# Kernel optimization log

Measured on AMD Instinct MI355X. Metric: run time of the kernel, lower is better.

Reference implementation:

```python
import jax, jax.numpy as jnp
import numpy as np

B = 2048; N_UP = 8; N_DN = 8; N_EL = 16; N_ION = 4
DF_EE = 4; DF_EI = 4; DF_II = 4; D_EL = 32; D_ION = 32
W_EDGE = 64; D_NODE = 128; CUTOFF = 5.0  # cutoff_distance, cutoff_type='exponential'


def setup_inputs() -> dict:
    key = jax.random.key(0)
    keys = iter(jax.random.split(key, 64))
    nk = lambda: next(keys)
    W = lambda fi, fo: jax.random.normal(nk(), (fi, fo), jnp.float32) / np.float32(np.sqrt(fi))
    b = lambda fo: jnp.zeros((fo,), jnp.float32)
    inp = {}
    inp["feat_el"] = jax.random.normal(nk(), (B, N_EL, D_EL), jnp.float32)
    inp["feat_el_el"] = jax.random.normal(nk(), (B, N_EL, N_EL, DF_EE), jnp.float32)
    inp["feat_el_ion"] = jax.random.normal(nk(), (B, N_EL, N_ION, DF_EI), jnp.float32)
    inp["feat_ion"] = jax.random.normal(nk(), (N_ION, D_ION), jnp.float32)
    inp["feat_ion_ion"] = jax.random.normal(nk(), (N_ION, N_ION, DF_II), jnp.float32)
    inp["dist_el_el"] = jax.random.uniform(nk(), (B, N_EL, N_EL), jnp.float32) * 6.0 + 0.1
    inp["dist_el_ion"] = jax.random.uniform(nk(), (B, N_EL, N_ION), jnp.float32) * 6.0 + 0.1
    # 2-layer edge MLPs: el_ion, same-spin, diff-spin, ion_ion
    for p, fi in (("ei", DF_EI), ("sa", DF_EE), ("di", DF_EE), ("io", DF_II)):
        inp["W" + p + "0"] = W(fi, W_EDGE); inp["b" + p + "0"] = b(W_EDGE)
        inp["W" + p + "1"] = W(W_EDGE, W_EDGE); inp["b" + p + "1"] = b(W_EDGE)
    # el_ion message-passing layer
    inp["Ws_ei"] = W(D_ION, W_EDGE); inp["bs_ei"] = b(W_EDGE)
    inp["Wu_ei"] = W(D_EL + W_EDGE, D_NODE); inp["bu_ei"] = b(D_NODE)
    inp["We_ei"] = W(W_EDGE, W_EDGE); inp["be_ei"] = b(W_EDGE)
    # el_el dense GNN, 2 iterations
    for i in ("0", "1"):
        inp["Ws" + i] = W(D_NODE, W_EDGE); inp["bs" + i] = b(W_EDGE)
        inp["Wu" + i] = W(D_NODE + W_EDGE, D_NODE); inp["bu" + i] = b(D_NODE)
        inp["We" + i] = W(W_EDGE, W_EDGE); inp["be" + i] = b(W_EDGE)
    inp["n_up"] = N_UP
    return inp


def _mlp2(x, W0, b0, W1, b1):
    # MLP with linear_out=False -> activation on every layer
    return jnp.tanh(jnp.tanh(x @ W0 + b0) @ W1 + b1)


def _mp(x_r, x_s, e, mask, Ws, bs, Wu, bu, We, be):
    # Message passing: edge * projected-sender messages, masked sum over senders,
    # node update from [receiver, aggregated msg]; edge update by linear+tanh.
    s = jnp.tanh(x_s @ Ws + bs)                      # [..., n_s, De]
    msg = e * s[..., None, :, :] * mask[..., None]   # [..., n_r, n_s, De]
    agg = msg.sum(axis=-2)                           # [..., n_r, De]
    x_new = jnp.tanh(jnp.concatenate([x_r, agg], axis=-1) @ Wu + bu)
    e_new = jnp.tanh(e @ We + be)
    return x_new, e_new


def reference(feat_el, feat_el_el, feat_el_ion, feat_ion, feat_ion_ion, dist_el_el, dist_el_ion,
              Wei0, bei0, Wei1, bei1, Wsa0, bsa0, Wsa1, bsa1, Wdi0, bdi0, Wdi1, bdi1,
              Wio0, bio0, Wio1, bio1, Ws_ei, bs_ei, Wu_ei, bu_ei, We_ei, be_ei,
              Ws0, bs0, Wu0, bu0, We0, be0, Ws1, bs1, Wu1, bu1, We1, be1, n_up):
    n_el = feat_el.shape[-2]; n_dn = n_el - n_up
    bd = feat_el_el.shape[:-3]
    ee = feat_el_el
    # --- _embed_edges: slice el-el pairs into same/diff spin blocks ---
    up_up = ee[..., :n_up, :n_up, :].reshape(bd + (n_up * n_up, -1))
    up_dn = ee[..., :n_up, n_up:, :].reshape(bd + (n_up * n_dn, -1))
    dn_up = ee[..., n_up:, :n_up, :].reshape(bd + (n_dn * n_up, -1))
    dn_dn = ee[..., n_up:, n_up:, :].reshape(bd + (n_dn * n_dn, -1))
    same = _mlp2(jnp.concatenate([up_up, dn_dn], axis=-2), Wsa0, bsa0, Wsa1, bsa1)
    diff = _mlp2(jnp.concatenate([up_dn, dn_up], axis=-2), Wdi0, bdi0, Wdi1, bdi1)
    edge_el_ion = _mlp2(feat_el_ion, Wei0, bei0, Wei1, bei1)
    _edge_ion_ion = _mlp2(feat_ion_ion, Wio0, bio0, Wio1, bio1)  # unused when ion_gnn='none' (as in original)
    # --- reassemble el-el edges ---
    up_up = same[..., : n_up * n_up, :].reshape(bd + (n_up, n_up, -1))
    dn_dn = same[..., n_up * n_up :, :].reshape(bd + (n_dn, n_dn, -1))
    up_dn = diff[..., : n_up * n_dn, :].reshape(bd + (n_up, n_dn, -1))
    dn_up = diff[..., n_up * n_dn :, :].reshape(bd + (n_dn, n_up, -1))
    edge_el_el = jnp.concatenate([
        jnp.concatenate([up_up, up_dn], axis=-2),
        jnp.concatenate([dn_up, dn_dn], axis=-2)], axis=-3)
    # --- distance masks (cutoff_type='exponential') ---
    mask_ei = jnp.exp(-dist_el_ion / CUTOFF)
    mask_ee = jnp.exp(-dist_el_el / CUTOFF)
    # --- ion_gnn='none': emb_ion = raw ion features ---
    emb_ion = feat_ion
    # --- el-ion message passing, then 2-iteration dense el-el GNN ---
    emb_el, edge_el_ion = _mp(feat_el, emb_ion, edge_el_ion, mask_ei, Ws_ei, bs_ei, Wu_ei, bu_ei, We_ei, be_ei)
    emb_el, edge_el_el = _mp(emb_el, emb_el, edge_el_el, mask_ee, Ws0, bs0, Wu0, bu0, We0, be0)
    emb_el, edge_el_el = _mp(emb_el, emb_el, edge_el_el, mask_ee, Ws1, bs1, Wu1, bu1, We1, be1)
    return emb_el, feat_ion, edge_el_el, edge_el_ion
```

## Files before the change

### kernel.cpp

```cpp
#include <hip/hip_runtime.h>

typedef unsigned short u16;
typedef unsigned int u32;
typedef __attribute__((ext_vector_type(4))) unsigned int u32x4;
typedef __attribute__((ext_vector_type(2))) unsigned int u32x2;
typedef __attribute__((ext_vector_type(8))) short bf16x8;
typedef __attribute__((ext_vector_type(4))) float f32x4;

#define OFF_Wsa1F 0
#define OFF_Wdi1F 2048
#define OFF_Wei1F 4096
#define OFF_WeeiF 6144
#define OFF_We0F  8192
#define OFF_We1F  10240
#define OFF_Wsa0P 12288
#define OFF_Wdi0P 13312
#define OFF_Wei0P 14336
#define OFF_Ws0F  15360
#define OFF_Ws1F  23552
#define OFF_WueiF 31744
#define OFF_Wu0F  44032
#define OFF_Wu1F  68608
#define OFF_SION  93184
__device__ u32 g_frags[93440];

#define OUT_EMB 0
#define OUT_ION 4194304
#define OUT_EE  4194432
#define OUT_EI  37748864

__device__ __forceinline__ float lo2f(u32 v) { return __uint_as_float(v << 16); }
__device__ __forceinline__ float hi2f(u32 v) { return __uint_as_float(v & 0xffff0000u); }
__device__ __forceinline__ u16 f2bf(float f) {
  u32 u = __float_as_uint(f);
  u32 r = (u + 0x7fffu + ((u >> 16) & 1u)) >> 16;
  return (u16)r;
}
__device__ __forceinline__ u32 pack2(float a, float b) {
  return (u32)f2bf(a) | ((u32)f2bf(b) << 16);
}
__device__ __forceinline__ u32 split2(float x) {
  const u32 h = (u32)f2bf(x);
  const float hf = __uint_as_float(h << 16);
  return h | ((u32)f2bf(x - hf) << 16);
}
__device__ __forceinline__ float tfast(float x) {
  x = fminf(fmaxf(x, -15.f), 15.f);
  float e = __expf(2.f * x);
  return (e - 1.f) * __builtin_amdgcn_rcpf(e + 1.f);
}

#define MFMA(a, b, c) __builtin_amdgcn_mfma_f32_16x16x32_bf16( \
    __builtin_bit_cast(bf16x8, a), __builtin_bit_cast(bf16x8, b), c, 0, 0, 0)

__global__ void prep_kernel(const float* __restrict__ Wsa1, const float* __restrict__ Wdi1,
                            const float* __restrict__ Wei1, const float* __restrict__ Weei,
                            const float* __restrict__ We0, const float* __restrict__ We1,
                            const float* __restrict__ Wsa0, const float* __restrict__ Wdi0,
                            const float* __restrict__ Wei0,
                            const float* __restrict__ Ws0, const float* __restrict__ Ws1,
                            const float* __restrict__ Wuei,
                            const float* __restrict__ Wu0, const float* __restrict__ Wu1) {
  const int t = blockIdx.x * blockDim.x + threadIdx.x;
  const int T = gridDim.x * blockDim.x;
  const float* s64[6] = {Wsa1, Wdi1, Wei1, Weei, We0, We1};
  const float* sL1[3] = {Wsa0, Wdi0, Wei0};
#pragma unroll 1
  for (int idx = t; idx < 93184; idx += T) {
    u32 val;
    if (idx < 12288) {
      const int m = idx >> 11, r = idx & 2047;
      const int w = r & 3, lane = (r >> 2) & 63, tk = r >> 8;
      const int c = (tk >> 1) * 16 + (lane & 15);
      const int k = (tk & 1) * 32 + (lane >> 4) * 8 + w * 2;
      const float* W = s64[m];
      val = pack2(W[k * 64 + c], W[(k + 1) * 64 + c]);
    } else if (idx < 15360) {
      const int i2 = idx - 12288;
      const int m = i2 >> 10, r = i2 & 1023;
      const int w = r & 3, lane = (r >> 2) & 63, mt = r >> 8;
      const int c = mt * 16 + (lane & 15);
      const int k = (lane >> 4) * 8 + w * 2;
      const float* W = sL1[m];
      val = (k < 4) ? pack2(W[k * 64 + c], W[(k + 1) * 64 + c]) : 0u;
    } else if (idx < 31744) {
      const int i2 = idx - 15360;
      const float* W = (i2 < 8192) ? Ws0 : Ws1;
      const int r = i2 & 8191;
      const int w = r & 3, lane = (r >> 2) & 63, f = r >> 8;
      const int c = (f >> 3) * 16 + (lane & 15);
      const int ko = (f & 7) * 16 + ((lane >> 4) << 2) + w;
      const float v = W[ko * 64 + c];
      val = pack2(v, v);
    } else if (idx < 44032) {
      const int i2 = idx - 31744;
      const int w = i2 & 3, lane = (i2 >> 2) & 63, f = i2 >> 8;
      const int d = (f / 6) * 16 + (lane & 15);
      const int ko = (f % 6) * 16 + ((lane >> 4) << 2) + w;
      const float v = Wuei[ko * 128 + d];
      val = pack2(v, v);
    } else {
      const int i2 = idx - 44032;
      const float* W = (i2 < 24576) ? Wu0 : Wu1;
      const int r = (i2 < 24576) ? i2 : i2 - 24576;
      const int w = r & 3, lane = (r >> 2) & 63, f = r >> 8;
      const int d = (f / 12) * 16 + (lane & 15);
      const int ko = (f % 12) * 16 + ((lane >> 4) << 2) + w;
      const float v = W[ko * 128 + d];
      val = pack2(v, v);
    }
    g_frags[idx] = val;
  }
}

__global__ void sion_kernel(const float* __restrict__ fion, const float* __restrict__ Wsei,
                            const float* __restrict__ bsei, float* __restrict__ out) {
  const int t = threadIdx.x;
  if (t < 128) out[OUT_ION + t] = fion[t];
  const int i = t >> 6, c = t & 63;
  float acc = bsei[c];
  for (int k = 0; k < 32; ++k)
    acc += fion[i * 32 + k] * Wsei[k * 64 + c];
  ((float*)g_frags)[OFF_SION + i * 64 + c] = tfast(acc);
}

struct GP {
  const float *__restrict__ fel; const float *__restrict__ fee; const float *__restrict__ fei;
  const float *__restrict__ dee; const float *__restrict__ dei;
  const float *__restrict__ Wsa0; const float *__restrict__ Wdi0; const float *__restrict__ Wei0;
  const float *__restrict__ bsa0; const float *__restrict__ bsa1;
  const float *__restrict__ bdi0; const float *__restrict__ bdi1;
  const float *__restrict__ bei0; const float *__restrict__ bei1;
  const float *__restrict__ buei; const float *__restrict__ beei;
  const float *__restrict__ bs0; const float *__restrict__ bu0; const float *__restrict__ be0;
  const float *__restrict__ bs1; const float *__restrict__ bu1; const float *__restrict__ be1;
  float *__restrict__ out;
};

__device__ __forceinline__ void ee_gemm64(u32* s_ee, const u32* __restrict__ Wf,
                                          const float* __restrict__ bias,
                                          int wvu, int ln) {
  const int lhi = ln >> 4, llo = ln & 15;
  u32x4 af[4][2];
#pragma unroll
  for (int mt = 0; mt < 4; ++mt)
#pragma unroll
    for (int kt = 0; kt < 2; ++kt)
      af[mt][kt] = *(const u32x4*)(Wf + ((mt * 2 + kt) * 64 + ln) * 4);
#pragma unroll
  for (int nt = 0; nt < 2; ++nt) {
    const int rowe = wvu * 32 + nt * 16 + llo;
    const int sw = (rowe & 7) << 2;
    u32x4 bf[2];
#pragma unroll
    for (int kt = 0; kt < 2; ++kt)
      bf[kt] = *(const u32x4*)&s_ee[rowe * 32 + ((kt * 16 + lhi * 4) ^ sw)];
    f32x4 acc[4];
#pragma unroll
    for (int mt = 0; mt < 4; ++mt) {
      const float4 bv = *(const float4*)(bias + mt * 16 + lhi * 4);
      acc[mt] = f32x4{bv.x, bv.y, bv.z, bv.w};
    }
#pragma unroll
    for (int kt = 0; kt < 2; ++kt)
#pragma unroll
      for (int mt = 0; mt < 4; ++mt)
        acc[mt] = MFMA(af[mt][kt], bf[kt], acc[mt]);
#pragma unroll
    for (int mt = 0; mt < 4; ++mt) {
      u32x2 o;
      o.x = pack2(tfast(acc[mt].x), tfast(acc[mt].y));
      o.y = pack2(tfast(acc[mt].z), tfast(acc[mt].w));
      *(u32x2*)&s_ee[rowe * 32 + ((mt * 8 + lhi * 2) ^ sw)] = o;
    }
  }
}

__device__ __forceinline__ void ei_gemm64(u32* s_ei, const u32* __restrict__ Wf,
                                          const float* __restrict__ bias,
                                          int wvu, int ln) {
  const int nt = wvu & 3, mh = wvu >> 2;
  const int lhi = ln >> 4, llo = ln & 15;
  const int rowe = nt * 16 + llo;
  const int sw = (rowe & 7) << 2;
  u32x4 bfr[2], af[2][2];
#pragma unroll
  for (int kt = 0; kt < 2; ++kt)
    bfr[kt] = *(const u32x4*)&s_ei[rowe * 32 + ((kt * 16 + lhi * 4) ^ sw)];
#pragma unroll
  for (int m2 = 0; m2 < 2; ++m2)
#pragma unroll
    for (int kt = 0; kt < 2; ++kt)
      af[m2][kt] = *(const u32x4*)(Wf + (((mh * 2 + m2) * 2 + kt) * 64 + ln) * 4);
  __syncthreads();
#pragma unroll
  for (int m2 = 0; m2 < 2; ++m2) {
    const int mt = mh * 2 + m2;
    const float4 bv = *(const float4*)(bias + mt * 16 + lhi * 4);
    f32x4 acc = f32x4{bv.x, bv.y, bv.z, bv.w};
#pragma unroll
    for (int kt = 0; kt < 2; ++kt)
      acc = MFMA(af[m2][kt], bfr[kt], acc);
    u32x2 o;
    o.x = pack2(tfast(acc.x), tfast(acc.y));
    o.y = pack2(tfast(acc.z), tfast(acc.w));
    *(u32x2*)&s_ei[rowe * 32 + ((mt * 8 + lhi * 2) ^ sw)] = o;
  }
}

__global__ __launch_bounds__(512, 4) void gnn_kernel(GP g) {
  const int b = blockIdx.x;
  const int t = threadIdx.x;
  const int ln = t & 63;
  const int wvu = __builtin_amdgcn_readfirstlane(t >> 6);
  const int lhi = ln >> 4, llo = ln & 15;
  const u32* __restrict__ wsu = g_frags;

  __shared__ __align__(16) u32 s_ee[256 * 32];
  __shared__ __align__(16) u32 s_ei[64 * 32];
  __shared__ __align__(16) u32 s_pool[3072];
  __shared__ __align__(16) u32 s_agg[16 * 64];
  __shared__ __align__(16) u32 s_xel[16 * 32];
  __shared__ float s_mee[256];
  __shared__ float s_mei[64];
  u32* s_emb  = s_pool;
  u32* s_nd   = s_pool + 2048;

  if (t < 256) {
    s_mee[t] = __expf(g.dee[b * 256 + t] * -0.2f);
  } else {
    const int u = t - 256;
    const int r = u >> 4, w = u & 15;
    const float2 f2 = *(const float2*)(g.fel + b * 512 + r * 32 + w * 2);
    u32x2 sx; sx.x = split2(f2.x); sx.y = split2(f2.y);
    *(u32x2*)&s_xel[r * 32 + ((2 * w) ^ ((r & 7) << 2))] = sx;
    if (u < 64) s_mei[u] = __expf(g.dei[b * 64 + u] * -0.2f);
  }
  __syncthreads();

  {
    const int q = wvu >> 1, h = wvu & 1;
    const int i_el = ((q >> 1) << 3) + (ln >> 3);
    const int j_el = ((q & 1) << 3) + (ln & 7);
    const int row = q * 64 + ln;
    const bool same = (q == 0) || (q == 3);
    const float* __restrict__ W0 = same ? g.Wsa0 : g.Wdi0;
    const float* __restrict__ b0 = same ? g.bsa0 : g.bdi0;
    const float4 xv = *(const float4*)(g.fee + (size_t)(b * 256 + i_el * 16 + j_el) * 4);
    const int sw = (ln & 7) << 2;
#pragma unroll
    for (int u = 0; u < 4; ++u) {
      u32x4 hv;
#pragma unroll
      for (int p2 = 0; p2 < 4; ++p2) {
        const int c = h * 32 + u * 8 + p2 * 2;
        const float v0 = tfast(b0[c] + xv.x * W0[c] + xv.y * W0[64 + c] +
                               xv.z * W0[128 + c] + xv.w * W0[192 + c]);
        const float v1 = tfast(b0[c + 1] + xv.x * W0[c + 1] + xv.y * W0[64 + c + 1] +
                               xv.z * W0[128 + c + 1] + xv.w * W0[192 + c + 1]);
        hv[p2] = pack2(v0, v1);
      }
      *(u32x4*)&s_ee[row * 32 + ((h * 16 + u * 4) ^ sw)] = hv;
    }
  }
  {
    const int e = ln;
    const float4 xv = *(const float4*)(g.fei + (size_t)(b * 64 + e) * 4);
    u32x4 hv;
#pragma unroll
    for (int p2 = 0; p2 < 4; ++p2) {
      const int c = wvu * 8 + p2 * 2;
      const float v0 = tfast(g.bei0[c] + xv.x * g.Wei0[c] + xv.y * g.Wei0[64 + c] +
                             xv.z * g.Wei0[128 + c] + xv.w * g.Wei0[192 + c]);
      const float v1 = tfast(g.bei0[c + 1] + xv.x * g.Wei0[c + 1] + xv.y * g.Wei0[64 + c + 1] +
                             xv.z * g.Wei0[128 + c + 1] + xv.w * g.Wei0[192 + c + 1]);
      hv[p2] = pack2(v0, v1);
    }
    *(u32x4*)&s_ei[e * 32 + ((wvu * 4) ^ ((e & 7) << 2))] = hv;
  }
  __syncthreads();

  {
    const int q = wvu >> 1;
    const bool same = (q == 0) || (q == 3);
    ee_gemm64(s_ee, wsu + (same ? OFF_Wsa1F : OFF_Wdi1F), same ? g.bsa1 : g.bdi1, wvu, ln);
  }
  ei_gemm64(s_ei, wsu + OFF_Wei1F, g.bei1, wvu, ln);
  __syncthreads();

  {
    const int c2i = t & 31;
    const int r = t >> 5;
    const float* __restrict__ sion = (const float*)g_frags + OFF_SION;
    float a0 = 0.f, a1 = 0.f;
#pragma unroll
    for (int i = 0; i < 4; ++i) {
      const int row = r * 4 + i;
      const u32 ev = s_ei[row * 32 + (c2i ^ ((row & 7) << 2))];
      const float2 si = *(const float2*)(sion + i * 64 + c2i * 2);
      const float mk = s_mei[row];
      a0 += lo2f(ev) * si.x * mk;
      a1 += hi2f(ev) * si.y * mk;
    }
    u32x2 o; o.x = split2(a0); o.y = split2(a1);
    *(u32x2*)&s_agg[r * 64 + ((2 * c2i) ^ ((r & 7) << 2))] = o;
  }
  __syncthreads();

  {
    const int mt = wvu;
    const int sw = (llo & 7) << 2;
    u32x4 bfr[6];
    bfr[0] = *(const u32x4*)&s_xel[llo * 32 + ((lhi * 4) ^ sw)];
    bfr[1] = *(const u32x4*)&s_xel[llo * 32 + ((16 + lhi * 4) ^ sw)];
#pragma unroll
    for (int k2 = 0; k2 < 4; ++k2)
      bfr[2 + k2] = *(const u32x4*)&s_agg[llo * 64 + ((k2 * 16 + lhi * 4) ^ sw)];
    const float4 bv = *(const float4*)(g.buei + mt * 16 + lhi * 4);
    f32x4 acc = f32x4{bv.x, bv.y, bv.z, bv.w};
#pragma unroll
    for (int kt = 0; kt < 6; ++kt)
      acc = MFMA(*(const u32x4*)(wsu + OFF_WueiF + (mt * 6 + kt) * 256 + ln * 4),
                 bfr[kt], acc);
    u32x4 o;
    o[0] = split2(tfast(acc.x)); o[1] = split2(tfast(acc.y));
    o[2] = split2(tfast(acc.z)); o[3] = split2(tfast(acc.w));
    *(u32x4*)&s_emb[llo * 128 + ((mt * 16 + lhi * 4) ^ sw)] = o;
  }

  ei_gemm64(s_ei, wsu + OFF_WeeiF, g.beei, wvu, ln);
  __syncthreads();

  {
    float2* o = (float2*)(g.out + OUT_EI + (size_t)b * 4096);
#pragma unroll
    for (int ii = 0; ii < 4; ++ii) {
      const int iw = ii * 512 + t;
      const int row = iw >> 5, w = iw & 31;
      const u32 v = s_ei[row * 32 + (w ^ ((row & 7) << 2))];
      o[iw] = make_float2(lo2f(v), hi2f(v));
    }
  }

#pragma unroll 1
  for (int it = 0; it < 2; ++it) {
    const u32* __restrict__ Wsf = wsu + (it ? OFF_Ws1F : OFF_Ws0F);
    const u32* __restrict__ Wuf = wsu + (it ? OFF_Wu1F : OFF_Wu0F);
    const u32* __restrict__ WeF = wsu + (it ? OFF_We1F : OFF_We0F);
    const float* __restrict__ bs = it ? g.bs1 : g.bs0;
    const float* __restrict__ bu = it ? g.bu1 : g.bu0;
    const float* __restrict__ be = it ? g.be1 : g.be0;

    if (wvu < 4) {
      const int mt = wvu;
      const int sw = (llo & 7) << 2;
      const float4 bv = *(const float4*)(bs + mt * 16 + lhi * 4);
      f32x4 acc = f32x4{bv.x, bv.y, bv.z, bv.w};
#pragma unroll
      for (int kt = 0; kt < 8; ++kt) {
        const u32x4 bf = *(const u32x4*)&s_emb[llo * 128 + ((kt * 16 + lhi * 4) ^ sw)];
        const u32x4 af = *(const u32x4*)(Wsf + (mt * 8 + kt) * 256 + ln * 4);
        acc = MFMA(af, bf, acc);
      }
      u32x4 o;
      o[0] = split2(tfast(acc.x)); o[1] = split2(tfast(acc.y));
      o[2] = split2(tfast(acc.z)); o[3] = split2(tfast(acc.w));
      *(u32x4*)&s_nd[llo * 64 + ((mt * 16 + lhi * 4) ^ sw)] = o;
    }
    __syncthreads();

    {
      const int c2i = t & 31;
      const int r = t >> 5;
      const int rbase = ((r >> 3) << 7) + ((r & 7) << 3);
      float a0 = 0.f, a1 = 0.f;
#pragma unroll
      for (int s = 0; s < 16; ++s) {
        const int row = rbase + ((s >> 3) << 6) + (s & 7);
        const int swz = (s & 7) << 2;
        const u32 ev = s_ee[row * 32 + (c2i ^ swz)];
        const u32x2 nv = *(const u32x2*)&s_nd[s * 64 + ((2 * c2i) ^ swz)];
        const float mk = s_mee[r * 16 + s];
        a0 += lo2f(ev) * (lo2f(nv.x) + hi2f(nv.x)) * mk;
        a1 += hi2f(ev) * (lo2f(nv.y) + hi2f(nv.y)) * mk;
      }
      u32x2 o; o.x = split2(a0); o.y = split2(a1);
      *(u32x2*)&s_agg[r * 64 + ((2 * c2i) ^ ((r & 7) << 2))] = o;
    }
    __syncthreads();

    u32x4 embf[8], aggf[4];
    {
      const int sw = (llo & 7) << 2;
#pragma unroll
      for (int kt = 0; kt < 8; ++kt)
        embf[kt] = *(const u32x4*)&s_emb[llo * 128 + ((kt * 16 + lhi * 4) ^ sw)];
#pragma unroll
      for (int k2 = 0; k2 < 4; ++k2)
        aggf[k2] = *(const u32x4*)&s_agg[llo * 64 + ((k2 * 16 + lhi * 4) ^ sw)];
    }
    __syncthreads();
    {
      const int mt = wvu;
      const float4 bv = *(const float4*)(bu + mt * 16 + lhi * 4);
      f32x4 acc = f32x4{bv.x, bv.y, bv.z, bv.w};
#pragma unroll
      for (int kt = 0; kt < 8; ++kt)
        acc = MFMA(*(const u32x4*)(Wuf + (mt * 12 + kt) * 256 + ln * 4), embf[kt], acc);
#pragma unroll
      for (int k2 = 0; k2 < 4; ++k2)
        acc = MFMA(*(const u32x4*)(Wuf + (mt * 12 + 8 + k2) * 256 + ln * 4), aggf[k2], acc);
      const float v0 = tfast(acc.x), v1 = tfast(acc.y), v2 = tfast(acc.z), v3 = tfast(acc.w);
      if (it == 1)
        *(float4*)(g.out + OUT_EMB + (size_t)b * 2048 + llo * 128 + mt * 16 + lhi * 4) =
            make_float4(v0, v1, v2, v3);
      u32x4 o;
      o[0] = split2(v0); o[1] = split2(v1); o[2] = split2(v2); o[3] = split2(v3);
      const int sw = (llo & 7) << 2;
      *(u32x4*)&s_emb[llo * 128 + ((mt * 16 + lhi * 4) ^ sw)] = o;
    }

    ee_gemm64(s_ee, WeF, be, wvu, ln);
    __syncthreads();
  }

  {
    float2* o = (float2*)(g.out + OUT_EE + (size_t)b * 16384);
#pragma unroll 1
    for (int ii = 0; ii < 16; ++ii) {
      const int iw = ii * 512 + t;
      const int row = iw >> 5, w = iw & 31;
      const u32 v = s_ee[row * 32 + (w ^ ((row & 7) << 2))];
      const int i_el = (((row >> 7) & 1) << 3) | ((row >> 3) & 7);
      const int j_el = (((row >> 6) & 1) << 3) | (row & 7);
      o[(i_el * 16 + j_el) * 32 + w] = make_float2(lo2f(v), hi2f(v));
    }
  }
}

extern "C" void kernel_launch(void* const* d_in, const int* in_sizes, int n_in,
                              void* d_out, int out_size, void* d_ws, size_t ws_size,
                              hipStream_t stream) {
  (void)in_sizes; (void)n_in; (void)out_size; (void)d_ws; (void)ws_size;
  GP g;
  g.fel  = (const float*)d_in[0];
  g.fee  = (const float*)d_in[1];
  g.fei  = (const float*)d_in[2];
  const float* fion = (const float*)d_in[3];
  g.dee  = (const float*)d_in[5];
  g.dei  = (const float*)d_in[6];

  g.Wei0 = (const float*)d_in[7];  g.bei0 = (const float*)d_in[8];
  const float* Wei1 = (const float*)d_in[9];  g.bei1 = (const float*)d_in[10];
  g.Wsa0 = (const float*)d_in[11]; g.bsa0 = (const float*)d_in[12];
  const float* Wsa1 = (const float*)d_in[13]; g.bsa1 = (const float*)d_in[14];
  g.Wdi0 = (const float*)d_in[15]; g.bdi0 = (const float*)d_in[16];
  const float* Wdi1 = (const float*)d_in[17]; g.bdi1 = (const float*)d_in[18];
  const float* Wsei = (const float*)d_in[23];
  const float* bsei = (const float*)d_in[24];
  const float* Wuei = (const float*)d_in[25]; g.buei = (const float*)d_in[26];
  const float* Weei = (const float*)d_in[27]; g.beei = (const float*)d_in[28];
  const float* Ws0  = (const float*)d_in[29]; g.bs0  = (const float*)d_in[30];
  const float* Wu0  = (const float*)d_in[31]; g.bu0  = (const float*)d_in[32];
  const float* We0  = (const float*)d_in[33]; g.be0  = (const float*)d_in[34];
  const float* Ws1  = (const float*)d_in[35]; g.bs1  = (const float*)d_in[36];
  const float* Wu1  = (const float*)d_in[37]; g.bu1  = (const float*)d_in[38];
  const float* We1  = (const float*)d_in[39]; g.be1  = (const float*)d_in[40];

  g.out = (float*)d_out;

  hipLaunchKernelGGL(prep_kernel, dim3(64), dim3(256), 0, stream,
                     Wsa1, Wdi1, Wei1, Weei, We0, We1,
                     (const float*)d_in[11], (const float*)d_in[15], (const float*)d_in[7],
                     Ws0, Ws1, Wuei, Wu0, Wu1);
  hipLaunchKernelGGL(sion_kernel, dim3(1), dim3(256), 0, stream,
                     fion, Wsei, bsei, g.out);
  hipLaunchKernelGGL(gnn_kernel, dim3(2048), dim3(512), 0, stream, g);
}
```

Before: 388.3 us.

## Drop split-bf16 for aggregated messages and sender projections, vectorize output stores

Aggregated messages and sender-projected node features are now stored as single bf16 instead of hi/lo split pairs. This halves the K dimension of the update GEMMs that consume them and shrinks the weight fragment tables and LDS buffers. It also replaces software bf16 rounding with the v_cvt_pk_bf16_f32 instruction, keeps the distance masks in registers instead of LDS, and widens the output stores to float4. The cost is lower precision on the aggregation inputs and more per-thread registers for the mask values.

```diff
diff --git a/kernel.cpp b/kernel.cpp
--- a/kernel.cpp
+++ b/kernel.cpp
@@ -13,16 +13,13 @@
 #define OFF_WeeiF 6144
 #define OFF_We0F  8192
 #define OFF_We1F  10240
-#define OFF_Wsa0P 12288
-#define OFF_Wdi0P 13312
-#define OFF_Wei0P 14336
-#define OFF_Ws0F  15360
-#define OFF_Ws1F  23552
-#define OFF_WueiF 31744
-#define OFF_Wu0F  44032
-#define OFF_Wu1F  68608
-#define OFF_SION  93184
-__device__ u32 g_frags[93440];
+#define OFF_Ws0F  12288
+#define OFF_Ws1F  20480
+#define OFF_WueiF 28672
+#define OFF_Wu0F  36864
+#define OFF_Wu1F  57344
+#define OFF_SION  77824
+__device__ u32 g_frags[78080];
 
 #define OUT_EMB 0
 #define OUT_ION 4194304
@@ -31,18 +28,18 @@
 
 __device__ __forceinline__ float lo2f(u32 v) { return __uint_as_float(v << 16); }
 __device__ __forceinline__ float hi2f(u32 v) { return __uint_as_float(v & 0xffff0000u); }
-__device__ __forceinline__ u16 f2bf(float f) {
-  u32 u = __float_as_uint(f);
-  u32 r = (u + 0x7fffu + ((u >> 16) & 1u)) >> 16;
-  return (u16)r;
-}
 __device__ __forceinline__ u32 pack2(float a, float b) {
-  return (u32)f2bf(a) | ((u32)f2bf(b) << 16);
+  u32 r;
+  asm("v_cvt_pk_bf16_f32 %0, %1, %2" : "=v"(r) : "v"(a), "v"(b));
+  return r;
 }
 __device__ __forceinline__ u32 split2(float x) {
-  const u32 h = (u32)f2bf(x);
+  u32 h;
+  asm("v_cvt_pk_bf16_f32 %0, %1, 0" : "=v"(h) : "v"(x));
   const float hf = __uint_as_float(h << 16);
-  return h | ((u32)f2bf(x - hf) << 16);
+  u32 r;
+  asm("v_cvt_pk_bf16_f32 %0, %1, %2" : "=v"(r) : "v"(x), "v"(x - hf));
+  return r;
 }
 __device__ __forceinline__ float tfast(float x) {
   x = fminf(fmaxf(x, -15.f), 15.f);
@@ -56,17 +53,14 @@
 __global__ void prep_kernel(const float* __restrict__ Wsa1, const float* __restrict__ Wdi1,
                             const float* __restrict__ Wei1, const float* __restrict__ Weei,
                             const float* __restrict__ We0, const float* __restrict__ We1,
-                            const float* __restrict__ Wsa0, const float* __restrict__ Wdi0,
-                            const float* __restrict__ Wei0,
                             const float* __restrict__ Ws0, const float* __restrict__ Ws1,
                             const float* __restrict__ Wuei,
                             const float* __restrict__ Wu0, const float* __restrict__ Wu1) {
   const int t = blockIdx.x * blockDim.x + threadIdx.x;
   const int T = gridDim.x * blockDim.x;
   const float* s64[6] = {Wsa1, Wdi1, Wei1, Weei, We0, We1};
-  const float* sL1[3] = {Wsa0, Wdi0, Wei0};
 #pragma unroll 1
-  for (int idx = t; idx < 93184; idx += T) {
+  for (int idx = t; idx < 77824; idx += T) {
     u32 val;
     if (idx < 12288) {
       const int m = idx >> 11, r = idx & 2047;
@@ -75,16 +69,8 @@
       const int k = (tk & 1) * 32 + (lane >> 4) * 8 + w * 2;
       const float* W = s64[m];
       val = pack2(W[k * 64 + c], W[(k + 1) * 64 + c]);
-    } else if (idx < 15360) {
+    } else if (idx < 28672) {
       const int i2 = idx - 12288;
-      const int m = i2 >> 10, r = i2 & 1023;
-      const int w = r & 3, lane = (r >> 2) & 63, mt = r >> 8;
-      const int c = mt * 16 + (lane & 15);
-      const int k = (lane >> 4) * 8 + w * 2;
-      const float* W = sL1[m];
-      val = (k < 4) ? pack2(W[k * 64 + c], W[(k + 1) * 64 + c]) : 0u;
-    } else if (idx < 31744) {
-      const int i2 = idx - 15360;
       const float* W = (i2 < 8192) ? Ws0 : Ws1;
       const int r = i2 & 8191;
       const int w = r & 3, lane = (r >> 2) & 63, f = r >> 8;
@@ -92,22 +78,34 @@
       const int ko = (f & 7) * 16 + ((lane >> 4) << 2) + w;
       const float v = W[ko * 64 + c];
       val = pack2(v, v);
-    } else if (idx < 44032) {
-      const int i2 = idx - 31744;
+    } else if (idx < 36864) {
+      const int i2 = idx - 28672;
       const int w = i2 & 3, lane = (i2 >> 2) & 63, f = i2 >> 8;
-      const int d = (f / 6) * 16 + (lane & 15);
-      const int ko = (f % 6) * 16 + ((lane >> 4) << 2) + w;
-      const float v = Wuei[ko * 128 + d];
-      val = pack2(v, v);
+      const int mt = f >> 2, kt = f & 3;
+      const int d = mt * 16 + (lane & 15);
+      if (kt < 2) {
+        const int ko = kt * 16 + ((lane >> 4) << 2) + w;
+        const float v = Wuei[ko * 128 + d];
+        val = pack2(v, v);
+      } else {
+        const int k = (kt - 2) * 32 + (lane >> 4) * 8 + w * 2;
+        val = pack2(Wuei[(32 + k) * 128 + d], Wuei[(33 + k) * 128 + d]);
+      }
     } else {
-      const int i2 = idx - 44032;
-      const float* W = (i2 < 24576) ? Wu0 : Wu1;
-      const int r = (i2 < 24576) ? i2 : i2 - 24576;
+      const int i2 = idx - 36864;
+      const float* W = (i2 < 20480) ? Wu0 : Wu1;
+      const int r = (i2 < 20480) ? i2 : i2 - 20480;
       const int w = r & 3, lane = (r >> 2) & 63, f = r >> 8;
-      const int d = (f / 12) * 16 + (lane & 15);
-      const int ko = (f % 12) * 16 + ((lane >> 4) << 2) + w;
-      const float v = W[ko * 128 + d];
-      val = pack2(v, v);
+      const int mt = f / 10, kt = f % 10;
+      const int d = mt * 16 + (lane & 15);
+      if (kt < 8) {
+        const int ko = kt * 16 + ((lane >> 4) << 2) + w;
+        const float v = W[ko * 128 + d];
+        val = pack2(v, v);
+      } else {
+        const int k = (kt - 8) * 32 + (lane >> 4) * 8 + w * 2;
+        val = pack2(W[(128 + k) * 128 + d], W[(129 + k) * 128 + d]);
+      }
     }
     g_frags[idx] = val;
   }
@@ -218,23 +216,28 @@
 
   __shared__ __align__(16) u32 s_ee[256 * 32];
   __shared__ __align__(16) u32 s_ei[64 * 32];
-  __shared__ __align__(16) u32 s_pool[3072];
-  __shared__ __align__(16) u32 s_agg[16 * 64];
-  __shared__ __align__(16) u32 s_xel[16 * 32];
-  __shared__ float s_mee[256];
-  __shared__ float s_mei[64];
-  u32* s_emb  = s_pool;
-  u32* s_nd   = s_pool + 2048;
-
+  __shared__ __align__(16) u32 s_pool[2560];
+  __shared__ __align__(16) u32 s_agg[16 * 32];
+  u32* s_emb = s_pool;
+  u32* s_nx  = s_pool + 2048;
+
+  float mee[16];
+  {
+    const float4* dr = (const float4*)(g.dee + b * 256 + (t >> 5) * 16);
+#pragma unroll
+    for (int j4 = 0; j4 < 4; ++j4) {
+      const float4 d4 = dr[j4];
+      mee[j4 * 4 + 0] = __expf(d4.x * -0.2f);
+      mee[j4 * 4 + 1] = __expf(d4.y * -0.2f);
+      mee[j4 * 4 + 2] = __expf(d4.z * -0.2f);
+      mee[j4 * 4 + 3] = __expf(d4.w * -0.2f);
+    }
+  }
   if (t < 256) {
-    s_mee[t] = __expf(g.dee[b * 256 + t] * -0.2f);
-  } else {
-    const int u = t - 256;
-    const int r = u >> 4, w = u & 15;
+    const int r = t >> 4, w = t & 15;
     const float2 f2 = *(const float2*)(g.fel + b * 512 + r * 32 + w * 2);
     u32x2 sx; sx.x = split2(f2.x); sx.y = split2(f2.y);
-    *(u32x2*)&s_xel[r * 32 + ((2 * w) ^ ((r & 7) << 2))] = sx;
-    if (u < 64) s_mei[u] = __expf(g.dei[b * 64 + u] * -0.2f);
+    *(u32x2*)&s_nx[r * 32 + ((2 * w) ^ ((r & 7) << 2))] = sx;
   }
   __syncthreads();
 
@@ -289,38 +292,37 @@
   __syncthreads();
 
   {
-    const int c2i = t & 31;
-    const int r = t >> 5;
+    const int c2i = t & 31, r = t >> 5;
     const float* __restrict__ sion = (const float*)g_frags + OFF_SION;
+    const float4 di4 = *(const float4*)(g.dei + b * 64 + r * 4);
+    const float mk[4] = {__expf(di4.x * -0.2f), __expf(di4.y * -0.2f),
+                         __expf(di4.z * -0.2f), __expf(di4.w * -0.2f)};
     float a0 = 0.f, a1 = 0.f;
 #pragma unroll
     for (int i = 0; i < 4; ++i) {
       const int row = r * 4 + i;
       const u32 ev = s_ei[row * 32 + (c2i ^ ((row & 7) << 2))];
       const float2 si = *(const float2*)(sion + i * 64 + c2i * 2);
-      const float mk = s_mei[row];
-      a0 += lo2f(ev) * si.x * mk;
-      a1 += hi2f(ev) * si.y * mk;
-    }
-    u32x2 o; o.x = split2(a0); o.y = split2(a1);
-    *(u32x2*)&s_agg[r * 64 + ((2 * c2i) ^ ((r & 7) << 2))] = o;
+      a0 += lo2f(ev) * si.x * mk[i];
+      a1 += hi2f(ev) * si.y * mk[i];
+    }
+    s_agg[r * 32 + (c2i ^ ((r & 7) << 2))] = pack2(a0, a1);
   }
   __syncthreads();
 
   {
     const int mt = wvu;
     const int sw = (llo & 7) << 2;
-    u32x4 bfr[6];
-    bfr[0] = *(const u32x4*)&s_xel[llo * 32 + ((lhi * 4) ^ sw)];
-    bfr[1] = *(const u32x4*)&s_xel[llo * 32 + ((16 + lhi * 4) ^ sw)];
-#pragma unroll
-    for (int k2 = 0; k2 < 4; ++k2)
-      bfr[2 + k2] = *(const u32x4*)&s_agg[llo * 64 + ((k2 * 16 + lhi * 4) ^ sw)];
+    u32x4 bfr[4];
+    bfr[0] = *(const u32x4*)&s_nx[llo * 32 + ((lhi * 4) ^ sw)];
+    bfr[1] = *(const u32x4*)&s_nx[llo * 32 + ((16 + lhi * 4) ^ sw)];
+    bfr[2] = *(const u32x4*)&s_agg[llo * 32 + ((lhi * 4) ^ sw)];
+    bfr[3] = *(const u32x4*)&s_agg[llo * 32 + ((16 + lhi * 4) ^ sw)];
     const float4 bv = *(const float4*)(g.buei + mt * 16 + lhi * 4);
     f32x4 acc = f32x4{bv.x, bv.y, bv.z, bv.w};
 #pragma unroll
-    for (int kt = 0; kt < 6; ++kt)
-      acc = MFMA(*(const u32x4*)(wsu + OFF_WueiF + (mt * 6 + kt) * 256 + ln * 4),
+    for (int kt = 0; kt < 4; ++kt)
+      acc = MFMA(*(const u32x4*)(wsu + OFF_WueiF + (mt * 4 + kt) * 256 + ln * 4),
                  bfr[kt], acc);
     u32x4 o;
     o[0] = split2(tfast(acc.x)); o[1] = split2(tfast(acc.y));
@@ -332,13 +334,13 @@
   __syncthreads();
 
   {
-    float2* o = (float2*)(g.out + OUT_EI + (size_t)b * 4096);
-#pragma unroll
-    for (int ii = 0; ii < 4; ++ii) {
-      const int iw = ii * 512 + t;
-      const int row = iw >> 5, w = iw & 31;
-      const u32 v = s_ei[row * 32 + (w ^ ((row & 7) << 2))];
-      o[iw] = make_float2(lo2f(v), hi2f(v));
+    float4* o4 = (float4*)(g.out + OUT_EI + (size_t)b * 4096);
+#pragma unroll
+    for (int ii = 0; ii < 2; ++ii) {
+      const int iw2 = ii * 1024 + t * 2;
+      const int row = iw2 >> 5, w = iw2 & 31;
+      const u32x2 v = *(const u32x2*)&s_ei[row * 32 + (w ^ ((row & 7) << 2))];
+      o4[iw2 >> 1] = make_float4(lo2f(v.x), hi2f(v.x), lo2f(v.y), hi2f(v.y));
     }
   }
 
@@ -359,19 +361,17 @@
 #pragma unroll
       for (int kt = 0; kt < 8; ++kt) {
         const u32x4 bf = *(const u32x4*)&s_emb[llo * 128 + ((kt * 16 + lhi * 4) ^ sw)];
-        const u32x4 af = *(const u32x4*)(Wsf + (mt * 8 + kt) * 256 + ln * 4);
-        acc = MFMA(af, bf, acc);
+        acc = MFMA(*(const u32x4*)(Wsf + (mt * 8 + kt) * 256 + ln * 4), bf, acc);
       }
-      u32x4 o;
-      o[0] = split2(tfast(acc.x)); o[1] = split2(tfast(acc.y));
-      o[2] = split2(tfast(acc.z)); o[3] = split2(tfast(acc.w));
-      *(u32x4*)&s_nd[llo * 64 + ((mt * 16 + lhi * 4) ^ sw)] = o;
+      u32x2 o;
+      o.x = pack2(tfast(acc.x), tfast(acc.y));
+      o.y = pack2(tfast(acc.z), tfast(acc.w));
+      *(u32x2*)&s_nx[llo * 32 + ((mt * 8 + lhi * 2) ^ sw)] = o;
     }
     __syncthreads();
 
     {
-      const int c2i = t & 31;
-      const int r = t >> 5;
+      const int c2i = t & 31, r = t >> 5;
       const int rbase = ((r >> 3) << 7) + ((r & 7) << 3);
       float a0 = 0.f, a1 = 0.f;
 #pragma unroll
@@ -379,25 +379,22 @@
         const int row = rbase + ((s >> 3) << 6) + (s & 7);
         const int swz = (s & 7) << 2;
         const u32 ev = s_ee[row * 32 + (c2i ^ swz)];
-        const u32x2 nv = *(const u32x2*)&s_nd[s * 64 + ((2 * c2i) ^ swz)];
-        const float mk = s_mee[r * 16 + s];
-        a0 += lo2f(ev) * (lo2f(nv.x) + hi2f(nv.x)) * mk;
-        a1 += hi2f(ev) * (lo2f(nv.y) + hi2f(nv.y)) * mk;
+        const u32 nv = s_nx[s * 32 + (c2i ^ swz)];
+        a0 += lo2f(ev) * lo2f(nv) * mee[s];
+        a1 += hi2f(ev) * hi2f(nv) * mee[s];
       }
-      u32x2 o; o.x = split2(a0); o.y = split2(a1);
-      *(u32x2*)&s_agg[r * 64 + ((2 * c2i) ^ ((r & 7) << 2))] = o;
+      s_agg[r * 32 + (c2i ^ ((r & 7) << 2))] = pack2(a0, a1);
     }
     __syncthreads();
 
-    u32x4 embf[8], aggf[4];
+    u32x4 embf[8], aggf[2];
     {
       const int sw = (llo & 7) << 2;
 #pragma unroll
       for (int kt = 0; kt < 8; ++kt)
         embf[kt] = *(const u32x4*)&s_emb[llo * 128 + ((kt * 16 + lhi * 4) ^ sw)];
-#pragma unroll
-      for (int k2 = 0; k2 < 4; ++k2)
-        aggf[k2] = *(const u32x4*)&s_agg[llo * 64 + ((k2 * 16 + lhi * 4) ^ sw)];
+      aggf[0] = *(const u32x4*)&s_agg[llo * 32 + ((lhi * 4) ^ sw)];
+      aggf[1] = *(const u32x4*)&s_agg[llo * 32 + ((16 + lhi * 4) ^ sw)];
     }
     __syncthreads();
     {
@@ -406,10 +403,10 @@
       f32x4 acc = f32x4{bv.x, bv.y, bv.z, bv.w};
 #pragma unroll
       for (int kt = 0; kt < 8; ++kt)
-        acc = MFMA(*(const u32x4*)(Wuf + (mt * 12 + kt) * 256 + ln * 4), embf[kt], acc);
-#pragma unroll
-      for (int k2 = 0; k2 < 4; ++k2)
-        acc = MFMA(*(const u32x4*)(Wuf + (mt * 12 + 8 + k2) * 256 + ln * 4), aggf[k2], acc);
+        acc = MFMA(*(const u32x4*)(Wuf + (mt * 10 + kt) * 256 + ln * 4), embf[kt], acc);
+#pragma unroll
+      for (int k2 = 0; k2 < 2; ++k2)
+        acc = MFMA(*(const u32x4*)(Wuf + (mt * 10 + 8 + k2) * 256 + ln * 4), aggf[k2], acc);
       const float v0 = tfast(acc.x), v1 = tfast(acc.y), v2 = tfast(acc.z), v3 = tfast(acc.w);
       if (it == 1)
         *(float4*)(g.out + OUT_EMB + (size_t)b * 2048 + llo * 128 + mt * 16 + lhi * 4) =
@@ -425,15 +422,16 @@
   }
 
   {
-    float2* o = (float2*)(g.out + OUT_EE + (size_t)b * 16384);
+    float4* o4 = (float4*)(g.out + OUT_EE + (size_t)b * 16384);
 #pragma unroll 1
-    for (int ii = 0; ii < 16; ++ii) {
-      const int iw = ii * 512 + t;
-      const int row = iw >> 5, w = iw & 31;
-      const u32 v = s_ee[row * 32 + (w ^ ((row & 7) << 2))];
+    for (int ii = 0; ii < 8; ++ii) {
+      const int iw2 = ii * 1024 + t * 2;
+      const int row = iw2 >> 5, w = iw2 & 31;
+      const u32x2 v = *(const u32x2*)&s_ee[row * 32 + (w ^ ((row & 7) << 2))];
       const int i_el = (((row >> 7) & 1) << 3) | ((row >> 3) & 7);
       const int j_el = (((row >> 6) & 1) << 3) | (row & 7);
-      o[(i_el * 16 + j_el) * 32 + w] = make_float2(lo2f(v), hi2f(v));
+      o4[(i_el * 16 + j_el) * 16 + (w >> 1)] =
+          make_float4(lo2f(v.x), hi2f(v.x), lo2f(v.y), hi2f(v.y));
     }
   }
 }
@@ -471,7 +469,6 @@
 
   hipLaunchKernelGGL(prep_kernel, dim3(64), dim3(256), 0, stream,
                      Wsa1, Wdi1, Wei1, Weei, We0, We1,
-                     (const float*)d_in[11], (const float*)d_in[15], (const float*)d_in[7],
                      Ws0, Ws1, Wuei, Wu0, Wu1);
   hipLaunchKernelGGL(sion_kernel, dim3(1), dim3(256), 0, stream,
                      fion, Wsei, bsei, g.out);
```

Result: faster. 370.6 us (-4.5%).
